# Kernel optimization log

Measured on AMD Instinct MI355X. Metric: run time of the kernel, lower is better.

The kernel has to match this reference:

```python
import jax, jax.numpy as jnp
import numpy as np

B, T, S, D, F = 4, 2048, 2048, 256, 1024
EPS = 1e-5


def setup_inputs() -> dict:
    key = jax.random.key(0)
    ks = jax.random.split(key, 24)
    def lin(kw, kb, din, dout):
        w = jax.random.normal(kw, (din, dout), jnp.float32) / np.sqrt(din)
        b = jax.random.normal(kb, (dout,), jnp.float32) * 0.01
        return w, b
    Wq1, bq1 = lin(ks[0], ks[1], D, D)
    Wk1, bk1 = lin(ks[2], ks[3], D, D)
    Wv1, bv1 = lin(ks[4], ks[5], D, D)
    Wq2, bq2 = lin(ks[6], ks[7], D, D)
    Wk2, bk2 = lin(ks[8], ks[9], D, D)
    Wv2, bv2 = lin(ks[10], ks[11], D, D)
    W1, b1 = lin(ks[12], ks[13], D, F)
    W2, b2 = lin(ks[14], ks[15], F, D)
    y = jax.random.normal(ks[16], (B, T, D), jnp.float32)
    Z = jax.random.normal(ks[17], (B, S, D), jnp.float32)
    target_mask = jnp.tril(jnp.ones((T, T), jnp.int32))  # causal 0/1 mask
    return dict(y=y, Z=Z, target_mask=target_mask,
                Wq1=Wq1, bq1=bq1, Wk1=Wk1, bk1=bk1, Wv1=Wv1, bv1=bv1,
                Wq2=Wq2, bq2=bq2, Wk2=Wk2, bk2=bk2, Wv2=Wv2, bv2=bv2,
                W1=W1, b1=b1, W2=W2, b2=b2,
                g1=jnp.ones((D,), jnp.float32), be1=jnp.zeros((D,), jnp.float32),
                g2=jnp.ones((D,), jnp.float32), be2=jnp.zeros((D,), jnp.float32),
                g3=jnp.ones((D,), jnp.float32), be3=jnp.zeros((D,), jnp.float32))


def _ln(x, g, b):
    m = x.mean(-1, keepdims=True)
    v = ((x - m) ** 2).mean(-1, keepdims=True)
    return (x - m) / jnp.sqrt(v + EPS) * g + b


def _attn(Q, K, V, mask=None):
    scale = 1.0 / np.sqrt(Q.shape[-1]).astype(np.float32)
    scores = jnp.einsum('btd,bsd->bts', Q, K) * scale  # [B,T,S]
    if mask is not None:
        scores = jnp.where(mask == 0, -jnp.inf, scores)
    probs = jax.nn.softmax(scores, axis=-1)
    return jnp.einsum('bts,bsd->btd', probs, V)


def reference(y, Z, target_mask, Wq1, bq1, Wk1, bk1, Wv1, bv1,
              Wq2, bq2, Wk2, bk2, Wv2, bv2, W1, b1, W2, b2,
              g1, be1, g2, be2, g3, be3):
    # self attention
    sa = _attn(y @ Wq1 + bq1, y @ Wk1 + bk1, y @ Wv1 + bv1, target_mask)
    y1 = _ln(y + sa, g1, be1)
    # cross attention
    ca = _attn(y1 @ Wq2 + bq2, Z @ Wk2 + bk2, Z @ Wv2 + bv2)
    y2 = _ln(y1 + ca, g2, be2)
    # FFN
    ffn = jax.nn.relu(y2 @ W1 + b1) @ W2 + b2
    return _ln(y2 + ffn, g3, be3)
```

## Files before the change

kernel.cpp:

```cpp
#include <hip/hip_runtime.h>

#define B_ 4
#define T_ 2048
#define S_ 2048
#define D_ 256
#define F_ 1024

typedef unsigned short ushort_t;
typedef __bf16 v8bf __attribute__((ext_vector_type(8)));
typedef float v4f __attribute__((ext_vector_type(4)));
typedef __attribute__((address_space(1))) const unsigned int gas_uint;
typedef __attribute__((address_space(3))) unsigned int las_uint;

__device__ __forceinline__ ushort_t f2bf(float f) {
  unsigned u = __float_as_uint(f);
  unsigned r = (u + 0x7FFFu + ((u >> 16) & 1u)) >> 16;
  return (ushort_t)r;
}
__device__ __forceinline__ float bf2f(ushort_t u) {
  return __uint_as_float((unsigned)u << 16);
}

struct WP { const float* s; ushort_t* d; int K, N; };
struct WP8 { WP m[8]; };

__global__ void prep_weights_k(WP8 a) {
  WP w = a.m[blockIdx.z];
  int k0 = blockIdx.x * 64, n0 = blockIdx.y * 64;
  if (k0 >= w.K || n0 >= w.N) return;
  __shared__ ushort_t tile[64][65];
  int tx = threadIdx.x, ty = threadIdx.y;
  for (int r = ty; r < 64; r += 4)
    tile[r][tx] = f2bf(w.s[(size_t)(k0 + r) * w.N + n0 + tx]);
  __syncthreads();
  for (int r = ty; r < 64; r += 4)
    w.d[(size_t)(n0 + r) * w.K + k0 + tx] = tile[tx][r];
}

__global__ void pack_bias_k(const float* bq1, const float* bk1, const float* bv1,
                            const float* bk2, const float* bv2,
                            float* bqkv1, float* bkv2) {
  int t = blockIdx.x * 256 + threadIdx.x;
  if (t < 768) bqkv1[t] = (t < 256) ? bq1[t] : (t < 512) ? bk1[t - 256] : bv1[t - 512];
  if (t < 512) bkv2[t] = (t < 256) ? bk2[t] : bv2[t - 256];
}

__global__ void cvt_k(const float* __restrict__ a, ushort_t* __restrict__ oa,
                      const float* __restrict__ b, ushort_t* __restrict__ ob) {
  int i = blockIdx.x * 256 + threadIdx.x;
  const float* s = blockIdx.y ? b : a;
  ushort_t* d = blockIdx.y ? ob : oa;
  size_t off = (size_t)i * 8;
  float4 v0 = *(const float4*)(s + off);
  float4 v1 = *(const float4*)(s + off + 4);
  union { ushort_t u[8]; uint4 v; } pk;
  pk.u[0] = f2bf(v0.x); pk.u[1] = f2bf(v0.y); pk.u[2] = f2bf(v0.z); pk.u[3] = f2bf(v0.w);
  pk.u[4] = f2bf(v1.x); pk.u[5] = f2bf(v1.y); pk.u[6] = f2bf(v1.z); pk.u[7] = f2bf(v1.w);
  *(uint4*)(d + off) = pk.v;
}

__global__ void transpose_bf16_k(const ushort_t* __restrict__ in, long long sIz, int ldin,
                                 ushort_t* __restrict__ out, long long sOz,
                                 int rows, int cols) {
  in  += (size_t)blockIdx.z * sIz;
  out += (size_t)blockIdx.z * sOz;
  __shared__ ushort_t tile[64][65];
  int r0 = blockIdx.x * 64, c0 = blockIdx.y * 64;
  int tx = threadIdx.x, ty = threadIdx.y;
  for (int r = ty; r < 64; r += 4)
    tile[r][tx] = in[(size_t)(r0 + r) * ldin + c0 + tx];
  __syncthreads();
  for (int r = ty; r < 64; r += 4)
    out[(size_t)(c0 + r) * rows + r0 + tx] = tile[tx][r];
}

template<bool RELU>
__global__ __launch_bounds__(256, 2) void gemm_bt(
    const ushort_t* __restrict__ A, int lda, long long sAz,
    const ushort_t* __restrict__ Bt, int ldb, long long sBz,
    const float* __restrict__ bias,
    float* __restrict__ Cf, ushort_t* __restrict__ Cb, int ldc, long long sCz,
    int K, float alpha, int causal, int kcausal, int crow0) {
  const int n0 = blockIdx.x * 64, m0 = blockIdx.y * 128;
  if (causal && n0 > crow0 + m0 + 127) return;
  const int Keff = kcausal ? ((crow0 + m0 + 128 < K) ? crow0 + m0 + 128 : K) : K;
  A  += (long long)blockIdx.z * sAz;
  Bt += (long long)blockIdx.z * sBz;
  const long long coff = (long long)blockIdx.z * sCz;
  const int t = threadIdx.x, lane = t & 63, wv = t >> 6;
  const int wm = wv >> 1, wn = wv & 1;
  const int kslot = lane >> 4, l15 = lane & 15;
  __shared__ __align__(16) char smem[24576];
  char* sA = smem;
  char* sB = smem + 16384;

  v4f acc[4][2];
  v4f zero = {0.f, 0.f, 0.f, 0.f};
#pragma unroll
  for (int m = 0; m < 4; ++m)
#pragma unroll
    for (int n = 0; n < 2; ++n) acc[m][n] = zero;

  for (int kk = 0; kk < Keff; kk += 64) {
    __syncthreads();
#pragma unroll
    for (int q = 0; q < 4; ++q) {
      int g = q * 256 + t;
      int row = g >> 3, j = g & 7;
      const ushort_t* src = A + (long long)(m0 + row) * lda + kk + ((j ^ (row & 7)) << 3);
      __builtin_amdgcn_global_load_lds((gas_uint*)src,
          (las_uint*)(sA + q * 4096 + (wv << 10)), 16, 0, 0);
    }
#pragma unroll
    for (int q = 0; q < 2; ++q) {
      int g = q * 256 + t;
      int row = g >> 3, j = g & 7;
      const ushort_t* src = Bt + (long long)(n0 + row) * ldb + kk + ((j ^ (row & 7)) << 3);
      __builtin_amdgcn_global_load_lds((gas_uint*)src,
          (las_uint*)(sB + q * 4096 + (wv << 10)), 16, 0, 0);
    }
    __syncthreads();
#pragma unroll
    for (int ks = 0; ks < 2; ++ks) {
      v8bf af[4]; v8bf bfr[2];
#pragma unroll
      for (int m = 0; m < 4; ++m) {
        int row = wm * 64 + m * 16 + l15;
        int gs = (ks * 4 + kslot) ^ (row & 7);
        af[m] = *(const v8bf*)(sA + ((row * 8 + gs) << 4));
      }
#pragma unroll
      for (int n = 0; n < 2; ++n) {
        int row = wn * 32 + n * 16 + l15;
        int gs = (ks * 4 + kslot) ^ (row & 7);
        bfr[n] = *(const v8bf*)(sB + ((row * 8 + gs) << 4));
      }
#pragma unroll
      for (int m = 0; m < 4; ++m)
#pragma unroll
        for (int n = 0; n < 2; ++n)
          acc[m][n] = __builtin_amdgcn_mfma_f32_16x16x32_bf16(af[m], bfr[n], acc[m][n], 0, 0, 0);
    }
  }
#pragma unroll
  for (int m = 0; m < 4; ++m) {
    int grow0 = m0 + wm * 64 + m * 16 + (kslot << 2);
#pragma unroll
    for (int n = 0; n < 2; ++n) {
      int gcol = n0 + wn * 32 + n * 16 + l15;
      float bb = bias ? bias[gcol] : 0.f;
#pragma unroll
      for (int i = 0; i < 4; ++i) {
        float v = acc[m][n][i] * alpha + bb;
        if (RELU) v = fmaxf(v, 0.f);
        long long off = coff + (long long)(grow0 + i) * ldc + gcol;
        if (Cf) Cf[off] = v;
        if (Cb) Cb[off] = f2bf(v);
      }
    }
  }
}

template<bool RELU>
__global__ __launch_bounds__(256, 2) void gemm_bt128(
    const ushort_t* __restrict__ A, int lda, long long sAz,
    const ushort_t* __restrict__ Bt, int ldb, long long sBz,
    const float* __restrict__ bias,
    float* __restrict__ Cf, ushort_t* __restrict__ Cb, int ldc, long long sCz,
    int K, float alpha, int causal, int crow0) {
  const int n0 = blockIdx.x * 128, m0 = blockIdx.y * 128;
  if (causal && n0 > crow0 + m0 + 127) return;
  A  += (long long)blockIdx.z * sAz;
  Bt += (long long)blockIdx.z * sBz;
  const long long coff = (long long)blockIdx.z * sCz;
  const int t = threadIdx.x, lane = t & 63, wv = t >> 6;
  const int wm = wv >> 1, wn = wv & 1;
  const int kslot = lane >> 4, l15 = lane & 15;
  __shared__ __align__(16) char smem[32768];
  char* sA = smem;
  char* sB = smem + 16384;

  v4f acc[4][4];
  v4f zero = {0.f, 0.f, 0.f, 0.f};
#pragma unroll
  for (int m = 0; m < 4; ++m)
#pragma unroll
    for (int n = 0; n < 4; ++n) acc[m][n] = zero;

  for (int kk = 0; kk < K; kk += 64) {
    __syncthreads();
#pragma unroll
    for (int q = 0; q < 4; ++q) {
      int g = q * 256 + t;
      int row = g >> 3, j = g & 7;
      const ushort_t* src = A + (long long)(m0 + row) * lda + kk + ((j ^ (row & 7)) << 3);
      __builtin_amdgcn_global_load_lds((gas_uint*)src,
          (las_uint*)(sA + q * 4096 + (wv << 10)), 16, 0, 0);
    }
#pragma unroll
    for (int q = 0; q < 4; ++q) {
      int g = q * 256 + t;
      int row = g >> 3, j = g & 7;
      const ushort_t* src = Bt + (long long)(n0 + row) * ldb + kk + ((j ^ (row & 7)) << 3);
      __builtin_amdgcn_global_load_lds((gas_uint*)src,
          (las_uint*)(sB + q * 4096 + (wv << 10)), 16, 0, 0);
    }
    __syncthreads();
#pragma unroll
    for (int ks = 0; ks < 2; ++ks) {
      v8bf af[4]; v8bf bfr[4];
#pragma unroll
      for (int m = 0; m < 4; ++m) {
        int row = wm * 64 + m * 16 + l15;
        int gs = (ks * 4 + kslot) ^ (row & 7);
        af[m] = *(const v8bf*)(sA + ((row * 8 + gs) << 4));
      }
#pragma unroll
      for (int n = 0; n < 4; ++n) {
        int row = wn * 64 + n * 16 + l15;
        int gs = (ks * 4 + kslot) ^ (row & 7);
        bfr[n] = *(const v8bf*)(sB + ((row * 8 + gs) << 4));
      }
#pragma unroll
      for (int m = 0; m < 4; ++m)
#pragma unroll
        for (int n = 0; n < 4; ++n)
          acc[m][n] = __builtin_amdgcn_mfma_f32_16x16x32_bf16(af[m], bfr[n], acc[m][n], 0, 0, 0);
    }
  }
#pragma unroll
  for (int m = 0; m < 4; ++m) {
    int grow0 = m0 + wm * 64 + m * 16 + (kslot << 2);
#pragma unroll
    for (int n = 0; n < 4; ++n) {
      int gcol = n0 + wn * 64 + n * 16 + l15;
      float bb = bias ? bias[gcol] : 0.f;
#pragma unroll
      for (int i = 0; i < 4; ++i) {
        float v = acc[m][n][i] * alpha + bb;
        if (RELU) v = fmaxf(v, 0.f);
        long long off = coff + (long long)(grow0 + i) * ldc + gcol;
        if (Cf) Cf[off] = v;
        if (Cb) Cb[off] = f2bf(v);
      }
    }
  }
}

__global__ __launch_bounds__(256) void softmax_k(ushort_t* sc, int causal, int crow0) {
  int row = blockIdx.x;
  ushort_t* rp = sc + ((size_t)blockIdx.y * T_ + row) * S_;
  int t = threadIdx.x;
  int gr = crow0 + row;
  int vlim = causal ? gr + 1 : S_;
  int wlim = causal ? (((gr >> 7) + 1) << 7) : S_;
  if (wlim > S_) wlim = S_;
  float x[8];
  if (t * 8 < vlim) {
    union { ushort_t u[8]; uint4 v; } in;
    in.v = *(const uint4*)(rp + t * 8);
#pragma unroll
    for (int j = 0; j < 8; ++j) x[j] = bf2f(in.u[j]);
  } else {
#pragma unroll
    for (int j = 0; j < 8; ++j) x[j] = -3.0e38f;
  }
  float m = -3.0e38f;
#pragma unroll
  for (int j = 0; j < 8; ++j) if (t * 8 + j < vlim) m = fmaxf(m, x[j]);
  for (int mk = 1; mk < 64; mk <<= 1) m = fmaxf(m, __shfl_xor(m, mk));
  __shared__ float rbuf[8];
  if ((t & 63) == 0) rbuf[t >> 6] = m;
  __syncthreads();
  m = fmaxf(fmaxf(rbuf[0], rbuf[1]), fmaxf(rbuf[2], rbuf[3]));
  float p[8]; float l = 0.f;
#pragma unroll
  for (int j = 0; j < 8; ++j) { p[j] = (t * 8 + j < vlim) ? __expf(x[j] - m) : 0.f; l += p[j]; }
  for (int mk = 1; mk < 64; mk <<= 1) l += __shfl_xor(l, mk);
  if ((t & 63) == 0) rbuf[4 + (t >> 6)] = l;
  __syncthreads();
  l = rbuf[4] + rbuf[5] + rbuf[6] + rbuf[7];
  float inv = 1.f / l;
  if (t * 8 < wlim) {
    union { ushort_t u[8]; uint4 v; } pk;
#pragma unroll
    for (int j = 0; j < 8; ++j) pk.u[j] = f2bf(p[j] * inv);
    *(uint4*)(rp + t * 8) = pk.v;
  }
}

__global__ __launch_bounds__(256) void add_ln_k(
    const float* __restrict__ base, const float* __restrict__ delta,
    const float* __restrict__ g, const float* __restrict__ be,
    float* __restrict__ outf, ushort_t* __restrict__ outb) {
  int row = blockIdx.x * 4 + (threadIdx.x >> 6);
  int lane = threadIdx.x & 63;
  size_t off = (size_t)row * 256 + lane * 4;
  float4 xv = *(const float4*)(base + off);
  float4 dv = *(const float4*)(delta + off);
  float s0 = xv.x + dv.x, s1 = xv.y + dv.y, s2 = xv.z + dv.z, s3 = xv.w + dv.w;
  float sum = s0 + s1 + s2 + s3;
  for (int mk = 1; mk < 64; mk <<= 1) sum += __shfl_xor(sum, mk);
  float mean = sum * (1.f / 256.f);
  float e0 = s0 - mean, e1 = s1 - mean, e2 = s2 - mean, e3 = s3 - mean;
  float ss = e0 * e0 + e1 * e1 + e2 * e2 + e3 * e3;
  for (int mk = 1; mk < 64; mk <<= 1) ss += __shfl_xor(ss, mk);
  float rstd = rsqrtf(ss * (1.f / 256.f) + 1e-5f);
  float4 gv = *(const float4*)(g + lane * 4);
  float4 bv = *(const float4*)(be + lane * 4);
  float o0 = e0 * rstd * gv.x + bv.x, o1 = e1 * rstd * gv.y + bv.y;
  float o2 = e2 * rstd * gv.z + bv.z, o3 = e3 * rstd * gv.w + bv.w;
  float4 ov; ov.x = o0; ov.y = o1; ov.z = o2; ov.w = o3;
  *(float4*)(outf + off) = ov;
  if (outb) {
    union { ushort_t u[4]; uint2 v; } pk;
    pk.u[0] = f2bf(o0); pk.u[1] = f2bf(o1); pk.u[2] = f2bf(o2); pk.u[3] = f2bf(o3);
    *(uint2*)(outb + off) = pk.v;
  }
}

extern "C" void kernel_launch(void* const* d_in, const int* in_sizes, int n_in,
                              void* d_out, int out_size, void* d_ws, size_t ws_size,
                              hipStream_t stream) {
  const float* y   = (const float*)d_in[0];
  const float* Z   = (const float*)d_in[1];
  const float* Wq1 = (const float*)d_in[3];  const float* bq1 = (const float*)d_in[4];
  const float* Wk1 = (const float*)d_in[5];  const float* bk1 = (const float*)d_in[6];
  const float* Wv1 = (const float*)d_in[7];  const float* bv1 = (const float*)d_in[8];
  const float* Wq2 = (const float*)d_in[9];  const float* bq2 = (const float*)d_in[10];
  const float* Wk2 = (const float*)d_in[11]; const float* bk2 = (const float*)d_in[12];
  const float* Wv2 = (const float*)d_in[13]; const float* bv2 = (const float*)d_in[14];
  const float* W1  = (const float*)d_in[15]; const float* b1  = (const float*)d_in[16];
  const float* W2  = (const float*)d_in[17]; const float* b2  = (const float*)d_in[18];
  const float* g1  = (const float*)d_in[19]; const float* be1 = (const float*)d_in[20];
  const float* g2  = (const float*)d_in[21]; const float* be2 = (const float*)d_in[22];
  const float* g3  = (const float*)d_in[23]; const float* be3 = (const float*)d_in[24];
  float* out = (float*)d_out;

  char* p = (char*)d_ws;
  auto alloc = [&](size_t sz) { char* r = p; p += (sz + 255) & ~(size_t)255; return r; };
  const size_t NBT = (size_t)B_ * T_ * D_;
  ushort_t* Wq1t = (ushort_t*)alloc(D_ * D_ * 2);
  ushort_t* Wk1t = (ushort_t*)alloc(D_ * D_ * 2);
  ushort_t* Wv1t = (ushort_t*)alloc(D_ * D_ * 2);
  ushort_t* Wq2t = (ushort_t*)alloc(D_ * D_ * 2);
  ushort_t* Wk2t = (ushort_t*)alloc(D_ * D_ * 2);
  ushort_t* Wv2t = (ushort_t*)alloc(D_ * D_ * 2);
  ushort_t* W1t  = (ushort_t*)alloc((size_t)F_ * D_ * 2);
  ushort_t* W2t  = (ushort_t*)alloc((size_t)D_ * F_ * 2);
  float* bqkv1 = (float*)alloc(768 * 4);
  float* bkv2  = (float*)alloc(512 * 4);
  ushort_t* yb  = (ushort_t*)alloc(NBT * 2);
  ushort_t* Zb  = (ushort_t*)alloc(NBT * 2);
  float*    y1f = (float*)alloc(NBT * 4);
  ushort_t* y1b = (ushort_t*)alloc(NBT * 2);
  float*    y2f = (float*)alloc(NBT * 4);
  ushort_t* y2b = (ushort_t*)alloc(NBT * 2);
  ushort_t* QKVb = (ushort_t*)alloc((size_t)B_ * T_ * 768 * 2);
  ushort_t* Vt   = (ushort_t*)alloc(NBT * 2);
  ushort_t* Hb = QKVb;
  float* tmp = (float*)alloc(NBT * 4);
  ushort_t* sc = (ushort_t*)p;
  size_t remain = (ws_size > (size_t)(p - (char*)d_ws))
                      ? ws_size - (size_t)(p - (char*)d_ws) : 0;
  const size_t rowb = (size_t)S_ * 2;
  int CH = 0, TC = 0;
  if (remain >= (size_t)B_ * T_ * rowb)      { CH = B_; TC = T_; }
  else if (remain >= (size_t)T_ * rowb)      { CH = 1;  TC = T_; }
  else {
    int tc = (int)(remain / (rowb * 128)) * 128;
    if (tc > T_) tc = T_;
    CH = 1; TC = tc;
  }

  WP8 wp;
  wp.m[0] = {Wq1, Wq1t, D_, D_}; wp.m[1] = {Wk1, Wk1t, D_, D_};
  wp.m[2] = {Wv1, Wv1t, D_, D_}; wp.m[3] = {Wq2, Wq2t, D_, D_};
  wp.m[4] = {Wk2, Wk2t, D_, D_}; wp.m[5] = {Wv2, Wv2t, D_, D_};
  wp.m[6] = {W1, W1t, D_, F_};   wp.m[7] = {W2, W2t, F_, D_};
  prep_weights_k<<<dim3(16, 16, 8), dim3(64, 4), 0, stream>>>(wp);
  pack_bias_k<<<dim3(5), 256, 0, stream>>>(bq1, bk1, bv1, bk2, bv2, bqkv1, bkv2);
  cvt_k<<<dim3((int)(NBT / 8 / 256), 2), 256, 0, stream>>>(y, yb, Zb ? Z : Z, Zb);

  auto gemm = [&](const ushort_t* A, int lda, long long sAz,
                  const ushort_t* Bt, int ldb, long long sBz,
                  const float* bias, float* Cf, ushort_t* Cb, int ldc, long long sCz,
                  int M, int N, int K, float alpha, int causal, int kcausal,
                  bool relu, int Zn, int crow0, bool big) {
    if (big) {
      dim3 g(N / 128, M / 128, Zn);
      if (relu)
        gemm_bt128<true><<<g, 256, 0, stream>>>(A, lda, sAz, Bt, ldb, sBz, bias, Cf, Cb, ldc, sCz, K, alpha, causal, crow0);
      else
        gemm_bt128<false><<<g, 256, 0, stream>>>(A, lda, sAz, Bt, ldb, sBz, bias, Cf, Cb, ldc, sCz, K, alpha, causal, crow0);
    } else {
      dim3 g(N / 64, M / 128, Zn);
      if (relu)
        gemm_bt<true><<<g, 256, 0, stream>>>(A, lda, sAz, Bt, ldb, sBz, bias, Cf, Cb, ldc, sCz, K, alpha, causal, kcausal, crow0);
      else
        gemm_bt<false><<<g, 256, 0, stream>>>(A, lda, sAz, Bt, ldb, sBz, bias, Cf, Cb, ldc, sCz, K, alpha, causal, kcausal, crow0);
    }
  };

  auto attention = [&](float* attout, int causal) {
    transpose_bf16_k<<<dim3(S_ / 64, D_ / 64, B_), dim3(64, 4), 0, stream>>>(
        QKVb + 512, (long long)S_ * 768, 768, Vt, (long long)D_ * S_, S_, D_);
    if (TC <= 0) return;
    const ushort_t* Q = QKVb;
    const ushort_t* Kc = QKVb + 256;
    for (int b0 = 0; b0 < B_; b0 += CH) {
      for (int t0 = 0; t0 < T_; t0 += TC) {
        int rows = (t0 + TC <= T_) ? TC : (T_ - t0);
        gemm(Q + ((size_t)b0 * T_ + t0) * 768, 768, (long long)T_ * 768,
             Kc + (size_t)b0 * S_ * 768, 768, (long long)S_ * 768,
             nullptr, nullptr, sc, S_, (long long)T_ * S_,
             rows, S_, D_, 0.0625f, causal, 0, false, CH, t0, true);
        softmax_k<<<dim3(rows, CH), 256, 0, stream>>>(sc, causal, t0);
        gemm(sc, S_, (long long)T_ * S_,
             Vt + (size_t)b0 * D_ * S_, S_, (long long)D_ * S_,
             nullptr, attout + ((size_t)b0 * T_ + t0) * D_, nullptr, D_, (long long)T_ * D_,
             rows, D_, S_, 1.f, 0, causal, false, CH, t0, false);
      }
    }
  };

  gemm(yb, D_, 0, Wq1t, D_, 0, bqkv1, nullptr, QKVb, 768, 0,
       B_ * T_, 768, D_, 1.f, 0, 0, false, 1, 0, true);
  attention(tmp, 1);
  add_ln_k<<<dim3(B_ * T_ / 4), 256, 0, stream>>>(y, tmp, g1, be1, y1f, y1b);

  gemm(y1b, D_, 0, Wq2t, D_, 0, bq2, nullptr, QKVb, 768, 0,
       B_ * T_, D_, D_, 1.f, 0, 0, false, 1, 0, false);
  gemm(Zb, D_, 0, Wk2t, D_, 0, bkv2, nullptr, QKVb + 256, 768, 0,
       B_ * S_, 512, D_, 1.f, 0, 0, false, 1, 0, true);
  attention(tmp, 0);
  add_ln_k<<<dim3(B_ * T_ / 4), 256, 0, stream>>>(y1f, tmp, g2, be2, y2f, y2b);

  gemm(y2b, D_, 0, W1t, D_, 0, b1, nullptr, Hb, F_, 0,
       B_ * T_, F_, D_, 1.f, 0, 0, true, 1, 0, true);
  gemm(Hb, F_, 0, W2t, F_, 0, b2, tmp, nullptr, D_, 0,
       B_ * T_, D_, F_, 1.f, 0, 0, false, 1, 0, false);
  add_ln_k<<<dim3(B_ * T_ / 4), 256, 0, stream>>>(y2f, tmp, g3, be3, out, nullptr);
}
```

Measured before the change: 343.3 us.

## Fuse residual+LayerNorm into PV/FFN2 GEMMs and batch projection/prep launches

Adds a GEMM kernel that computes 32 full 256-wide output rows per block, then adds the bias and residual and applies LayerNorm in its epilogue. It replaces the separate add_ln passes after both attentions and the FFN, and removes the fp32 tmp round-trip. It also merges weight/input conversion into one launch, and computes the self-attention QKV and cross-attention K/V projections in a single two-slice launch with biases indexed inline. The V transposes for both attentions now run together up front. The PV GEMM now uses 32-row tiles with the full V^T slab staged in LDS, which lowers per-block reuse and occupancy. LayerNorm variance is taken as E[x²]−mean², which is less numerically robust.

```diff
diff --git a/kernel.cpp b/kernel.cpp
--- a/kernel.cpp
+++ b/kernel.cpp
@@ -24,46 +24,43 @@
 struct WP { const float* s; ushort_t* d; int K, N; };
 struct WP8 { WP m[8]; };
 
-__global__ void prep_weights_k(WP8 a) {
-  WP w = a.m[blockIdx.z];
-  int k0 = blockIdx.x * 64, n0 = blockIdx.y * 64;
-  if (k0 >= w.K || n0 >= w.N) return;
-  __shared__ ushort_t tile[64][65];
-  int tx = threadIdx.x, ty = threadIdx.y;
-  for (int r = ty; r < 64; r += 4)
-    tile[r][tx] = f2bf(w.s[(size_t)(k0 + r) * w.N + n0 + tx]);
-  __syncthreads();
-  for (int r = ty; r < 64; r += 4)
-    w.d[(size_t)(n0 + r) * w.K + k0 + tx] = tile[tx][r];
-}
-
-__global__ void pack_bias_k(const float* bq1, const float* bk1, const float* bv1,
-                            const float* bk2, const float* bv2,
-                            float* bqkv1, float* bkv2) {
-  int t = blockIdx.x * 256 + threadIdx.x;
-  if (t < 768) bqkv1[t] = (t < 256) ? bq1[t] : (t < 512) ? bk1[t - 256] : bv1[t - 512];
-  if (t < 512) bkv2[t] = (t < 256) ? bk2[t] : bv2[t - 256];
-}
-
-__global__ void cvt_k(const float* __restrict__ a, ushort_t* __restrict__ oa,
-                      const float* __restrict__ b, ushort_t* __restrict__ ob) {
-  int i = blockIdx.x * 256 + threadIdx.x;
-  const float* s = blockIdx.y ? b : a;
-  ushort_t* d = blockIdx.y ? ob : oa;
-  size_t off = (size_t)i * 8;
-  float4 v0 = *(const float4*)(s + off);
-  float4 v1 = *(const float4*)(s + off + 4);
-  union { ushort_t u[8]; uint4 v; } pk;
-  pk.u[0] = f2bf(v0.x); pk.u[1] = f2bf(v0.y); pk.u[2] = f2bf(v0.z); pk.u[3] = f2bf(v0.w);
-  pk.u[4] = f2bf(v1.x); pk.u[5] = f2bf(v1.y); pk.u[6] = f2bf(v1.z); pk.u[7] = f2bf(v1.w);
-  *(uint4*)(d + off) = pk.v;
-}
-
-__global__ void transpose_bf16_k(const ushort_t* __restrict__ in, long long sIz, int ldin,
-                                 ushort_t* __restrict__ out, long long sOz,
-                                 int rows, int cols) {
-  in  += (size_t)blockIdx.z * sIz;
-  out += (size_t)blockIdx.z * sOz;
+__global__ void prep_all_k(WP8 a, const float* __restrict__ y, ushort_t* __restrict__ yb,
+                           const float* __restrict__ Z, ushort_t* __restrict__ Zb) {
+  if (blockIdx.z < 8) {
+    WP w = a.m[blockIdx.z];
+    int k0 = blockIdx.x * 64, n0 = blockIdx.y * 64;
+    if (k0 >= w.K || n0 >= w.N) return;
+    __shared__ ushort_t tile[64][65];
+    int tx = threadIdx.x, ty = threadIdx.y;
+    for (int r = ty; r < 64; r += 4)
+      tile[r][tx] = f2bf(w.s[(size_t)(k0 + r) * w.N + n0 + tx]);
+    __syncthreads();
+    for (int r = ty; r < 64; r += 4)
+      w.d[(size_t)(n0 + r) * w.K + k0 + tx] = tile[tx][r];
+  } else {
+    int s = blockIdx.z - 8;
+    const float* src = (s >= 4) ? Z : y;
+    ushort_t* dst = (s >= 4) ? Zb : yb;
+    int lid = (s & 3) * 256 + blockIdx.y * 16 + blockIdx.x;
+    int tid = threadIdx.y * 64 + threadIdx.x;
+    size_t off = (size_t)lid * 2048 + (size_t)tid * 8;
+    float4 v0 = *(const float4*)(src + off);
+    float4 v1 = *(const float4*)(src + off + 4);
+    union { ushort_t u[8]; uint4 v; } pk;
+    pk.u[0] = f2bf(v0.x); pk.u[1] = f2bf(v0.y); pk.u[2] = f2bf(v0.z); pk.u[3] = f2bf(v0.w);
+    pk.u[4] = f2bf(v1.x); pk.u[5] = f2bf(v1.y); pk.u[6] = f2bf(v1.z); pk.u[7] = f2bf(v1.w);
+    *(uint4*)(dst + off) = pk.v;
+  }
+}
+
+__global__ void transpose_v_k(const ushort_t* __restrict__ V1, ushort_t* __restrict__ Vt1,
+                              const ushort_t* __restrict__ V2, ushort_t* __restrict__ Vt2) {
+  int z = blockIdx.z;
+  const ushort_t* in;
+  ushort_t* out;
+  int ldin;
+  if (z < 4) { in = V1 + (size_t)z * T_ * 768; out = Vt1 + (size_t)z * D_ * S_; ldin = 768; }
+  else       { in = V2 + (size_t)(z - 4) * S_ * 512; out = Vt2 + (size_t)(z - 4) * D_ * S_; ldin = 512; }
   __shared__ ushort_t tile[64][65];
   int r0 = blockIdx.x * 64, c0 = blockIdx.y * 64;
   int tx = threadIdx.x, ty = threadIdx.y;
@@ -71,7 +68,7 @@
     tile[r][tx] = in[(size_t)(r0 + r) * ldin + c0 + tx];
   __syncthreads();
   for (int r = ty; r < 64; r += 4)
-    out[(size_t)(c0 + r) * rows + r0 + tx] = tile[tx][r];
+    out[(size_t)(c0 + r) * S_ + r0 + tx] = tile[tx][r];
 }
 
 template<bool RELU>
@@ -247,6 +244,91 @@
   }
 }
 
+__global__ __launch_bounds__(256, 2) void gemm_proj(
+    const ushort_t* __restrict__ yb, const ushort_t* __restrict__ Zb,
+    const ushort_t* __restrict__ Wqkv1t, const ushort_t* __restrict__ Wkv2t,
+    ushort_t* __restrict__ QKVb, ushort_t* __restrict__ QKV2b,
+    const float* bq1, const float* bk1, const float* bv1,
+    const float* bk2, const float* bv2) {
+  const int z = blockIdx.z;
+  const int n0 = blockIdx.x * 128, m0 = blockIdx.y * 128;
+  if (z == 1 && n0 >= 512) return;
+  const ushort_t* A  = z ? Zb : yb;        const int lda = 256;
+  const ushort_t* Bt = z ? Wkv2t : Wqkv1t; const int ldb = 256;
+  ushort_t* Cb = z ? QKV2b : QKVb;         const int ldc = z ? 512 : 768;
+  const int t = threadIdx.x, lane = t & 63, wv = t >> 6;
+  const int wm = wv >> 1, wn = wv & 1;
+  const int kslot = lane >> 4, l15 = lane & 15;
+  __shared__ __align__(16) char smem[32768];
+  char* sA = smem;
+  char* sB = smem + 16384;
+
+  v4f acc[4][4];
+  v4f zero = {0.f, 0.f, 0.f, 0.f};
+#pragma unroll
+  for (int m = 0; m < 4; ++m)
+#pragma unroll
+    for (int n = 0; n < 4; ++n) acc[m][n] = zero;
+
+  for (int kk = 0; kk < 256; kk += 64) {
+    __syncthreads();
+#pragma unroll
+    for (int q = 0; q < 4; ++q) {
+      int g = q * 256 + t;
+      int row = g >> 3, j = g & 7;
+      const ushort_t* src = A + (long long)(m0 + row) * lda + kk + ((j ^ (row & 7)) << 3);
+      __builtin_amdgcn_global_load_lds((gas_uint*)src,
+          (las_uint*)(sA + q * 4096 + (wv << 10)), 16, 0, 0);
+    }
+#pragma unroll
+    for (int q = 0; q < 4; ++q) {
+      int g = q * 256 + t;
+      int row = g >> 3, j = g & 7;
+      const ushort_t* src = Bt + (long long)(n0 + row) * ldb + kk + ((j ^ (row & 7)) << 3);
+      __builtin_amdgcn_global_load_lds((gas_uint*)src,
+          (las_uint*)(sB + q * 4096 + (wv << 10)), 16, 0, 0);
+    }
+    __syncthreads();
+#pragma unroll
+    for (int ks = 0; ks < 2; ++ks) {
+      v8bf af[4]; v8bf bfr[4];
+#pragma unroll
+      for (int m = 0; m < 4; ++m) {
+        int row = wm * 64 + m * 16 + l15;
+        int gs = (ks * 4 + kslot) ^ (row & 7);
+        af[m] = *(const v8bf*)(sA + ((row * 8 + gs) << 4));
+      }
+#pragma unroll
+      for (int n = 0; n < 4; ++n) {
+        int row = wn * 64 + n * 16 + l15;
+        int gs = (ks * 4 + kslot) ^ (row & 7);
+        bfr[n] = *(const v8bf*)(sB + ((row * 8 + gs) << 4));
+      }
+#pragma unroll
+      for (int m = 0; m < 4; ++m)
+#pragma unroll
+        for (int n = 0; n < 4; ++n)
+          acc[m][n] = __builtin_amdgcn_mfma_f32_16x16x32_bf16(af[m], bfr[n], acc[m][n], 0, 0, 0);
+    }
+  }
+#pragma unroll
+  for (int m = 0; m < 4; ++m) {
+    int grow0 = m0 + wm * 64 + m * 16 + (kslot << 2);
+#pragma unroll
+    for (int n = 0; n < 4; ++n) {
+      int gcol = n0 + wn * 64 + n * 16 + l15;
+      float bb;
+      if (z == 0)
+        bb = (gcol < 256) ? bq1[gcol] : (gcol < 512) ? bk1[gcol - 256] : bv1[gcol - 512];
+      else
+        bb = (gcol < 256) ? bk2[gcol] : bv2[gcol - 256];
+#pragma unroll
+      for (int i = 0; i < 4; ++i)
+        Cb[(long long)(grow0 + i) * ldc + gcol] = f2bf(acc[m][n][i] + bb);
+    }
+  }
+}
+
 __global__ __launch_bounds__(256) void softmax_k(ushort_t* sc, int causal, int crow0) {
   int row = blockIdx.x;
   ushort_t* rp = sc + ((size_t)blockIdx.y * T_ + row) * S_;
@@ -289,34 +371,140 @@
   }
 }
 
-__global__ __launch_bounds__(256) void add_ln_k(
-    const float* __restrict__ base, const float* __restrict__ delta,
+template<int KCAUSAL>
+__global__ __launch_bounds__(256, 2) void pv_ln_k(
+    const ushort_t* __restrict__ A, int lda, long long sAz,
+    const ushort_t* __restrict__ Bt, int ldb, long long sBz,
+    const float* __restrict__ bias,
+    const float* __restrict__ base, long long sBasez,
     const float* __restrict__ g, const float* __restrict__ be,
-    float* __restrict__ outf, ushort_t* __restrict__ outb) {
-  int row = blockIdx.x * 4 + (threadIdx.x >> 6);
-  int lane = threadIdx.x & 63;
-  size_t off = (size_t)row * 256 + lane * 4;
-  float4 xv = *(const float4*)(base + off);
-  float4 dv = *(const float4*)(delta + off);
-  float s0 = xv.x + dv.x, s1 = xv.y + dv.y, s2 = xv.z + dv.z, s3 = xv.w + dv.w;
-  float sum = s0 + s1 + s2 + s3;
-  for (int mk = 1; mk < 64; mk <<= 1) sum += __shfl_xor(sum, mk);
-  float mean = sum * (1.f / 256.f);
-  float e0 = s0 - mean, e1 = s1 - mean, e2 = s2 - mean, e3 = s3 - mean;
-  float ss = e0 * e0 + e1 * e1 + e2 * e2 + e3 * e3;
-  for (int mk = 1; mk < 64; mk <<= 1) ss += __shfl_xor(ss, mk);
-  float rstd = rsqrtf(ss * (1.f / 256.f) + 1e-5f);
-  float4 gv = *(const float4*)(g + lane * 4);
-  float4 bv = *(const float4*)(be + lane * 4);
-  float o0 = e0 * rstd * gv.x + bv.x, o1 = e1 * rstd * gv.y + bv.y;
-  float o2 = e2 * rstd * gv.z + bv.z, o3 = e3 * rstd * gv.w + bv.w;
-  float4 ov; ov.x = o0; ov.y = o1; ov.z = o2; ov.w = o3;
-  *(float4*)(outf + off) = ov;
-  if (outb) {
-    union { ushort_t u[4]; uint2 v; } pk;
-    pk.u[0] = f2bf(o0); pk.u[1] = f2bf(o1); pk.u[2] = f2bf(o2); pk.u[3] = f2bf(o3);
-    *(uint2*)(outb + off) = pk.v;
-  }
+    float* __restrict__ outf, ushort_t* __restrict__ outb, long long sOz,
+    int K, int crow0) {
+  const int m0 = blockIdx.x * 32;
+  A  += (long long)blockIdx.z * sAz;
+  Bt += (long long)blockIdx.z * sBz;
+  const long long boff = (long long)blockIdx.z * sBasez;
+  const long long ooff = (long long)blockIdx.z * sOz;
+  const int t = threadIdx.x, lane = t & 63, wn = t >> 6;
+  const int kslot = lane >> 4, l15 = lane & 15;
+  __shared__ __align__(16) char sA[4096];
+  __shared__ __align__(16) char sB[32768];
+  __shared__ float sSum[32][4], sSq[32][4];
+
+  int Keff = K;
+  if (KCAUSAL) {
+    int kb = ((crow0 + m0 + 32 + 63) >> 6) << 6;
+    Keff = (kb < K) ? kb : K;
+  }
+
+  v4f acc[2][4];
+  v4f zero = {0.f, 0.f, 0.f, 0.f};
+#pragma unroll
+  for (int m = 0; m < 2; ++m)
+#pragma unroll
+    for (int n = 0; n < 4; ++n) acc[m][n] = zero;
+
+  for (int kk = 0; kk < Keff; kk += 64) {
+    __syncthreads();
+    {
+      int row = t >> 3, j = t & 7;
+      const ushort_t* src = A + (long long)(m0 + row) * lda + kk + ((j ^ (row & 7)) << 3);
+      __builtin_amdgcn_global_load_lds((gas_uint*)src,
+          (las_uint*)(sA + (wn << 10)), 16, 0, 0);
+    }
+#pragma unroll
+    for (int q = 0; q < 8; ++q) {
+      int gidx = q * 256 + t;
+      int row = gidx >> 3, j = gidx & 7;
+      const ushort_t* src = Bt + (long long)row * ldb + kk + ((j ^ (row & 7)) << 3);
+      __builtin_amdgcn_global_load_lds((gas_uint*)src,
+          (las_uint*)(sB + q * 4096 + (wn << 10)), 16, 0, 0);
+    }
+    __syncthreads();
+#pragma unroll
+    for (int ks = 0; ks < 2; ++ks) {
+      v8bf af[2]; v8bf bfr[4];
+#pragma unroll
+      for (int m = 0; m < 2; ++m) {
+        int row = m * 16 + l15;
+        int gs = (ks * 4 + kslot) ^ (row & 7);
+        af[m] = *(const v8bf*)(sA + ((row * 8 + gs) << 4));
+      }
+#pragma unroll
+      for (int n = 0; n < 4; ++n) {
+        int row = wn * 64 + n * 16 + l15;
+        int gs = (ks * 4 + kslot) ^ (row & 7);
+        bfr[n] = *(const v8bf*)(sB + ((row * 8 + gs) << 4));
+      }
+#pragma unroll
+      for (int m = 0; m < 2; ++m)
+#pragma unroll
+        for (int n = 0; n < 4; ++n)
+          acc[m][n] = __builtin_amdgcn_mfma_f32_16x16x32_bf16(af[m], bfr[n], acc[m][n], 0, 0, 0);
+    }
+  }
+
+  float sum[2][4], sq[2][4];
+#pragma unroll
+  for (int m = 0; m < 2; ++m)
+#pragma unroll
+    for (int i = 0; i < 4; ++i) { sum[m][i] = 0.f; sq[m][i] = 0.f; }
+#pragma unroll
+  for (int m = 0; m < 2; ++m)
+#pragma unroll
+    for (int n = 0; n < 4; ++n) {
+      int col = wn * 64 + n * 16 + l15;
+      float bb = bias ? bias[col] : 0.f;
+#pragma unroll
+      for (int i = 0; i < 4; ++i) {
+        int row = m0 + m * 16 + kslot * 4 + i;
+        float v = acc[m][n][i] + bb + base[boff + (long long)row * 256 + col];
+        acc[m][n][i] = v;
+        sum[m][i] += v;
+        sq[m][i] += v * v;
+      }
+    }
+#pragma unroll
+  for (int mk = 1; mk < 16; mk <<= 1) {
+#pragma unroll
+    for (int m = 0; m < 2; ++m)
+#pragma unroll
+      for (int i = 0; i < 4; ++i) {
+        sum[m][i] += __shfl_xor(sum[m][i], mk);
+        sq[m][i] += __shfl_xor(sq[m][i], mk);
+      }
+  }
+  if (l15 == 0) {
+#pragma unroll
+    for (int m = 0; m < 2; ++m)
+#pragma unroll
+      for (int i = 0; i < 4; ++i) {
+        int r = m * 16 + kslot * 4 + i;
+        sSum[r][wn] = sum[m][i];
+        sSq[r][wn] = sq[m][i];
+      }
+  }
+  __syncthreads();
+#pragma unroll
+  for (int m = 0; m < 2; ++m)
+#pragma unroll
+    for (int i = 0; i < 4; ++i) {
+      int r = m * 16 + kslot * 4 + i;
+      float s = sSum[r][0] + sSum[r][1] + sSum[r][2] + sSum[r][3];
+      float q2 = sSq[r][0] + sSq[r][1] + sSq[r][2] + sSq[r][3];
+      float mean = s * (1.f / 256.f);
+      float var = q2 * (1.f / 256.f) - mean * mean;
+      float rstd = rsqrtf(var + 1e-5f);
+      int row = m0 + r;
+#pragma unroll
+      for (int n = 0; n < 4; ++n) {
+        int col = wn * 64 + n * 16 + l15;
+        float o = (acc[m][n][i] - mean) * rstd * g[col] + be[col];
+        long long off = ooff + (long long)row * 256 + col;
+        outf[off] = o;
+        if (outb) outb[off] = f2bf(o);
+      }
+    }
 }
 
 extern "C" void kernel_launch(void* const* d_in, const int* in_sizes, int n_in,
@@ -348,18 +536,18 @@
   ushort_t* Wv2t = (ushort_t*)alloc(D_ * D_ * 2);
   ushort_t* W1t  = (ushort_t*)alloc((size_t)F_ * D_ * 2);
   ushort_t* W2t  = (ushort_t*)alloc((size_t)D_ * F_ * 2);
-  float* bqkv1 = (float*)alloc(768 * 4);
-  float* bkv2  = (float*)alloc(512 * 4);
   ushort_t* yb  = (ushort_t*)alloc(NBT * 2);
   ushort_t* Zb  = (ushort_t*)alloc(NBT * 2);
   float*    y1f = (float*)alloc(NBT * 4);
   ushort_t* y1b = (ushort_t*)alloc(NBT * 2);
   float*    y2f = (float*)alloc(NBT * 4);
   ushort_t* y2b = (ushort_t*)alloc(NBT * 2);
-  ushort_t* QKVb = (ushort_t*)alloc((size_t)B_ * T_ * 768 * 2);
-  ushort_t* Vt   = (ushort_t*)alloc(NBT * 2);
+  ushort_t* QKVb  = (ushort_t*)alloc((size_t)B_ * T_ * 768 * 2);
+  ushort_t* QKV2b = (ushort_t*)alloc((size_t)B_ * S_ * 512 * 2);
+  ushort_t* Qb  = (ushort_t*)alloc(NBT * 2);
+  ushort_t* Vt1 = (ushort_t*)alloc(NBT * 2);
+  ushort_t* Vt2 = (ushort_t*)alloc(NBT * 2);
   ushort_t* Hb = QKVb;
-  float* tmp = (float*)alloc(NBT * 4);
   ushort_t* sc = (ushort_t*)p;
   size_t remain = (ws_size > (size_t)(p - (char*)d_ws))
                       ? ws_size - (size_t)(p - (char*)d_ws) : 0;
@@ -378,67 +566,59 @@
   wp.m[2] = {Wv1, Wv1t, D_, D_}; wp.m[3] = {Wq2, Wq2t, D_, D_};
   wp.m[4] = {Wk2, Wk2t, D_, D_}; wp.m[5] = {Wv2, Wv2t, D_, D_};
   wp.m[6] = {W1, W1t, D_, F_};   wp.m[7] = {W2, W2t, F_, D_};
-  prep_weights_k<<<dim3(16, 16, 8), dim3(64, 4), 0, stream>>>(wp);
-  pack_bias_k<<<dim3(5), 256, 0, stream>>>(bq1, bk1, bv1, bk2, bv2, bqkv1, bkv2);
-  cvt_k<<<dim3((int)(NBT / 8 / 256), 2), 256, 0, stream>>>(y, yb, Zb ? Z : Z, Zb);
-
-  auto gemm = [&](const ushort_t* A, int lda, long long sAz,
-                  const ushort_t* Bt, int ldb, long long sBz,
-                  const float* bias, float* Cf, ushort_t* Cb, int ldc, long long sCz,
-                  int M, int N, int K, float alpha, int causal, int kcausal,
-                  bool relu, int Zn, int crow0, bool big) {
-    if (big) {
-      dim3 g(N / 128, M / 128, Zn);
-      if (relu)
-        gemm_bt128<true><<<g, 256, 0, stream>>>(A, lda, sAz, Bt, ldb, sBz, bias, Cf, Cb, ldc, sCz, K, alpha, causal, crow0);
-      else
-        gemm_bt128<false><<<g, 256, 0, stream>>>(A, lda, sAz, Bt, ldb, sBz, bias, Cf, Cb, ldc, sCz, K, alpha, causal, crow0);
-    } else {
-      dim3 g(N / 64, M / 128, Zn);
-      if (relu)
-        gemm_bt<true><<<g, 256, 0, stream>>>(A, lda, sAz, Bt, ldb, sBz, bias, Cf, Cb, ldc, sCz, K, alpha, causal, kcausal, crow0);
-      else
-        gemm_bt<false><<<g, 256, 0, stream>>>(A, lda, sAz, Bt, ldb, sBz, bias, Cf, Cb, ldc, sCz, K, alpha, causal, kcausal, crow0);
-    }
-  };
-
-  auto attention = [&](float* attout, int causal) {
-    transpose_bf16_k<<<dim3(S_ / 64, D_ / 64, B_), dim3(64, 4), 0, stream>>>(
-        QKVb + 512, (long long)S_ * 768, 768, Vt, (long long)D_ * S_, S_, D_);
+  prep_all_k<<<dim3(16, 16, 16), dim3(64, 4), 0, stream>>>(wp, y, yb, Z, Zb);
+
+  gemm_proj<<<dim3(6, 64, 2), 256, 0, stream>>>(yb, Zb, Wq1t, Wk2t, QKVb, QKV2b,
+                                                bq1, bk1, bv1, bk2, bv2);
+  transpose_v_k<<<dim3(S_ / 64, D_ / 64, 8), dim3(64, 4), 0, stream>>>(
+      QKVb + 512, Vt1, QKV2b + 256, Vt2);
+
+  auto attention = [&](const ushort_t* Q, int ldq, long long sQz,
+                       const ushort_t* Kc, int ldk, long long sKz,
+                       const ushort_t* Vt, const float* basef,
+                       const float* g, const float* be,
+                       float* outf, ushort_t* outb, int causal) {
     if (TC <= 0) return;
-    const ushort_t* Q = QKVb;
-    const ushort_t* Kc = QKVb + 256;
     for (int b0 = 0; b0 < B_; b0 += CH) {
       for (int t0 = 0; t0 < T_; t0 += TC) {
         int rows = (t0 + TC <= T_) ? TC : (T_ - t0);
-        gemm(Q + ((size_t)b0 * T_ + t0) * 768, 768, (long long)T_ * 768,
-             Kc + (size_t)b0 * S_ * 768, 768, (long long)S_ * 768,
-             nullptr, nullptr, sc, S_, (long long)T_ * S_,
-             rows, S_, D_, 0.0625f, causal, 0, false, CH, t0, true);
+        gemm_bt128<false><<<dim3(S_ / 128, rows / 128, CH), 256, 0, stream>>>(
+            Q + ((size_t)b0 * T_ + t0) * ldq, ldq, sQz,
+            Kc + (size_t)b0 * S_ * ldk, ldk, sKz,
+            nullptr, nullptr, sc, S_, (long long)T_ * S_,
+            D_, 0.0625f, causal, t0);
         softmax_k<<<dim3(rows, CH), 256, 0, stream>>>(sc, causal, t0);
-        gemm(sc, S_, (long long)T_ * S_,
-             Vt + (size_t)b0 * D_ * S_, S_, (long long)D_ * S_,
-             nullptr, attout + ((size_t)b0 * T_ + t0) * D_, nullptr, D_, (long long)T_ * D_,
-             rows, D_, S_, 1.f, 0, causal, false, CH, t0, false);
+        const float* basep = basef + ((size_t)b0 * T_ + t0) * 256;
+        float* outfp = outf + ((size_t)b0 * T_ + t0) * 256;
+        ushort_t* outbp = outb ? outb + ((size_t)b0 * T_ + t0) * 256 : nullptr;
+        if (causal)
+          pv_ln_k<1><<<dim3(rows / 32, 1, CH), 256, 0, stream>>>(
+              sc, S_, (long long)T_ * S_,
+              Vt + (size_t)b0 * D_ * S_, S_, (long long)D_ * S_,
+              nullptr, basep, (long long)T_ * 256, g, be,
+              outfp, outbp, (long long)T_ * 256, S_, t0);
+        else
+          pv_ln_k<0><<<dim3(rows / 32, 1, CH), 256, 0, stream>>>(
+              sc, S_, (long long)T_ * S_,
+              Vt + (size_t)b0 * D_ * S_, S_, (long long)D_ * S_,
+              nullptr, basep, (long long)T_ * 256, g, be,
+              outfp, outbp, (long long)T_ * 256, S_, t0);
       }
     }
   };
 
-  gemm(yb, D_, 0, Wq1t, D_, 0, bqkv1, nullptr, QKVb, 768, 0,
-       B_ * T_, 768, D_, 1.f, 0, 0, false, 1, 0, true);
-  attention(tmp, 1);
-  add_ln_k<<<dim3(B_ * T_ / 4), 256, 0, stream>>>(y, tmp, g1, be1, y1f, y1b);
-
-  gemm(y1b, D_, 0, Wq2t, D_, 0, bq2, nullptr, QKVb, 768, 0,
-       B_ * T_, D_, D_, 1.f, 0, 0, false, 1, 0, false);
-  gemm(Zb, D_, 0, Wk2t, D_, 0, bkv2, nullptr, QKVb + 256, 768, 0,
-       B_ * S_, 512, D_, 1.f, 0, 0, false, 1, 0, true);
-  attention(tmp, 0);
-  add_ln_k<<<dim3(B_ * T_ / 4), 256, 0, stream>>>(y1f, tmp, g2, be2, y2f, y2b);
-
-  gemm(y2b, D_, 0, W1t, D_, 0, b1, nullptr, Hb, F_, 0,
-       B_ * T_, F_, D_, 1.f, 0, 0, true, 1, 0, true);
-  gemm(Hb, F_, 0, W2t, F_, 0, b2, tmp, nullptr, D_, 0,
-       B_ * T_, D_, F_, 1.f, 0, 0, false, 1, 0, false);
-  add_ln_k<<<dim3(B_ * T_ / 4), 256, 0, stream>>>(y2f, tmp, g3, be3, out, nullptr);
-}
+  attention(QKVb, 768, (long long)T_ * 768, QKVb + 256, 768, (long long)S_ * 768,
+            Vt1, y, g1, be1, y1f, y1b, 1);
+
+  gemm_bt<false><<<dim3(D_ / 64, B_ * T_ / 128, 1), 256, 0, stream>>>(
+      y1b, D_, 0, Wq2t, D_, 0, bq2, nullptr, Qb, D_, 0, D_, 1.f, 0, 0, 0);
+
+  attention(Qb, 256, (long long)T_ * 256, QKV2b, 512, (long long)S_ * 512,
+            Vt2, y1f, g2, be2, y2f, y2b, 0);
+
+  gemm_bt128<true><<<dim3(F_ / 128, B_ * T_ / 128, 1), 256, 0, stream>>>(
+      y2b, D_, 0, W1t, D_, 0, b1, nullptr, Hb, F_, 0, D_, 1.f, 0, 0);
+
+  pv_ln_k<0><<<dim3(B_ * T_ / 32, 1, 1), 256, 0, stream>>>(
+      Hb, F_, 0, W2t, F_, 0, b2, y2f, 0, g3, be3, out, nullptr, 0, F_, 0);
+}
```

New measurement: 312.2 us. 1.1x faster.
